# Optimization experiments

Hardware: AMD Instinct MI355X
Metric: run time of the kernel (lower is better)

## Reference

```python
import jax, jax.numpy as jnp
import numpy as np

N = 8192
IN_C = 256
OUT_C = 64
ALPHA = 0.2  # LeakyReLU negative slope
NEG_INF = -9e15


def setup_inputs() -> dict:
    key = jax.random.key(0)
    k1, k2, k3, k4 = jax.random.split(key, 4)
    x = jax.random.normal(k1, (N, IN_C), dtype=jnp.float32)
    adjacent = jax.random.randint(k2, (N, N), 0, 2, dtype=jnp.int32)
    # xavier_uniform with gain=1.2: limit = gain * sqrt(6/(fan_in+fan_out))
    lim_w = 1.2 * np.sqrt(6.0 / (IN_C + OUT_C))
    w = jax.random.uniform(k3, (IN_C, OUT_C), dtype=jnp.float32, minval=-lim_w, maxval=lim_w)
    lim_a = 1.2 * np.sqrt(6.0 / (2 * OUT_C + 1))
    a = jax.random.uniform(k4, (2 * OUT_C, 1), dtype=jnp.float32, minval=-lim_a, maxval=lim_a)
    return {"x": x, "adjacent": adjacent, "w": w, "a": a}


def reference(x, adjacent, w, a):
    # h: [N, out]
    h = x @ w
    # e_ij = LeakyReLU(a^T [h_i || h_j]) computed without materializing [N,N,2*out]:
    # split a into source/target halves -> rank-1 broadcast sum.
    a_src = a[:OUT_C, 0]   # [out]
    a_dst = a[OUT_C:, 0]   # [out]
    f_src = h @ a_src      # [N]
    f_dst = h @ a_dst      # [N]
    e = f_src[:, None] + f_dst[None, :]            # [N, N]
    e = jnp.where(e > 0, e, ALPHA * e)             # LeakyReLU
    # mask by adjacency, softmax over neighbors (rows)
    e = jnp.where(adjacent > 0, e, NEG_INF)
    attention = jax.nn.softmax(e, axis=-1)         # [N, N]
    h_prime = attention @ h                        # [N, out]
    # concat=True -> ELU activation
    return jax.nn.elu(h_prime)
```

## Files before the change

### kernel.cpp

```cpp
#include <hip/hip_runtime.h>
#include <hip/hip_bf16.h>

#define N 8192
#define IN_C 256
#define OUT_C 64
#define ALPHA 0.2f

typedef short bf16x8 __attribute__((ext_vector_type(8)));
typedef float f32x4 __attribute__((ext_vector_type(4)));

#define OFF_H      0u
#define OFF_HT     2097152u
#define OFF_FS     3145728u
#define OFF_FD     3178496u
#define OFF_FDMAX  3211264u
#define OFF_NUM    3211520u

__global__ __launch_bounds__(256) void k_linear(const float* __restrict__ x,
                                                const float* __restrict__ w,
                                                const float* __restrict__ a,
                                                float* __restrict__ h,
                                                float* __restrict__ fs,
                                                float* __restrict__ fd) {
    __shared__ float wl[IN_C * OUT_C];
    int t = threadIdx.x;
    for (int idx = t; idx < IN_C * OUT_C; idx += 256) wl[idx] = w[idx];
    __syncthreads();
    int i = blockIdx.x * 4 + (t >> 6);
    int c = t & 63;
    const float* xr = x + (size_t)i * IN_C;
    float acc = 0.f;
#pragma unroll 8
    for (int k = 0; k < IN_C; ++k) acc = fmaf(xr[k], wl[k * 64 + c], acc);
    h[(size_t)i * 64 + c] = acc;
    float s = acc * a[c];
    float d = acc * a[64 + c];
#pragma unroll
    for (int off = 32; off > 0; off >>= 1) {
        s += __shfl_xor(s, off, 64);
        d += __shfl_xor(d, off, 64);
    }
    if (c == 0) { fs[i] = s; fd[i] = d; }
}

__global__ __launch_bounds__(256) void k_tr(const float* __restrict__ h,
                                            __hip_bfloat16* __restrict__ ht) {
    __shared__ __hip_bfloat16 lds[64 * 65];
    int t = threadIdx.x;
    int i0 = blockIdx.x * 64;
#pragma unroll
    for (int k = 0; k < 16; ++k) {
        int idx = k * 256 + t;
        int il = idx >> 6, c = idx & 63;
        lds[c * 65 + il] = __float2bfloat16(h[(size_t)(i0 + il) * 64 + c]);
    }
    __syncthreads();
#pragma unroll
    for (int k = 0; k < 16; ++k) {
        int idx = k * 256 + t;
        int c = idx >> 6, il = idx & 63;
        ht[(size_t)c * N + i0 + il] = lds[c * 65 + il];
    }
}

__global__ __launch_bounds__(256) void k_fdmax(const float* __restrict__ fd,
                                               float* __restrict__ out) {
    __shared__ float red[256];
    int t = threadIdx.x;
    float m = -3.4e38f;
    for (int j = t; j < N; j += 256) m = fmaxf(m, fd[j]);
    red[t] = m;
    __syncthreads();
    for (int s = 128; s > 0; s >>= 1) {
        if (t < s) red[t] = fmaxf(red[t], red[t + s]);
        __syncthreads();
    }
    if (t == 0) out[0] = red[0];
}

struct Stage {
    int4   ad0, ad1;
    float4 fd0, fd1;
    bf16x8 b0, b1, b2, b3;
};

__device__ __forceinline__ void load_stage(Stage& s,
        const int* __restrict__ arow, const float* __restrict__ fdst,
        const unsigned short* __restrict__ pb0, const unsigned short* __restrict__ pb1,
        const unsigned short* __restrict__ pb2, const unsigned short* __restrict__ pb3,
        int jb) {
    s.ad0 = *(const int4*)(arow + jb);
    s.ad1 = *(const int4*)(arow + jb + 4);
    s.fd0 = *(const float4*)(fdst + jb);
    s.fd1 = *(const float4*)(fdst + jb + 4);
    s.b0  = *(const bf16x8*)(pb0 + jb);
    s.b1  = *(const bf16x8*)(pb1 + jb);
    s.b2  = *(const bf16x8*)(pb2 + jb);
    s.b3  = *(const bf16x8*)(pb3 + jb);
}

__device__ __forceinline__ void compute_stage(const Stage& s, float fs, float m,
        float& dacc, f32x4& acc0, f32x4& acc1, f32x4& acc2, f32x4& acc3) {
    int   ad[8]  = {s.ad0.x, s.ad0.y, s.ad0.z, s.ad0.w, s.ad1.x, s.ad1.y, s.ad1.z, s.ad1.w};
    float fdv[8] = {s.fd0.x, s.fd0.y, s.fd0.z, s.fd0.w, s.fd1.x, s.fd1.y, s.fd1.z, s.fd1.w};
    bf16x8 af;
#pragma unroll
    for (int e = 0; e < 8; ++e) {
        float ee = fs + fdv[e];
        float l  = fmaxf(ee, ALPHA * ee);
        float wt = (ad[e] > 0) ? __expf(l - m) : 0.f;
        dacc += wt;
        union { float f; unsigned u; } cv; cv.f = wt;
        unsigned ru = cv.u + 0x7FFF + ((cv.u >> 16) & 1);
        af[e] = (short)(ru >> 16);
    }
    acc0 = __builtin_amdgcn_mfma_f32_16x16x32_bf16(af, s.b0, acc0, 0, 0, 0);
    acc1 = __builtin_amdgcn_mfma_f32_16x16x32_bf16(af, s.b1, acc1, 0, 0, 0);
    acc2 = __builtin_amdgcn_mfma_f32_16x16x32_bf16(af, s.b2, acc2, 0, 0, 0);
    acc3 = __builtin_amdgcn_mfma_f32_16x16x32_bf16(af, s.b3, acc3, 0, 0, 0);
}

__global__ __launch_bounds__(256) void k_main(
    const int* __restrict__ adj,
    const float* __restrict__ fsrc,
    const float* __restrict__ fdst,
    const float* __restrict__ fdmax_p,
    const unsigned short* __restrict__ ht,
    float* __restrict__ nump,
    float* __restrict__ denp_out,
    int jch, int ns) {
    int bid = blockIdx.x;
    int rb = bid & 127;
    int kq = bid >> 7;
    int t = threadIdx.x;
    int wave = t >> 6;
    int lane = t & 63;
    int r  = lane & 15;
    int kg = lane >> 4;
    int i  = rb * 64 + wave * 16 + r;
    int j0 = kq * jch;

    float fs  = fsrc[i];
    float fdm = *fdmax_p;
    float e0  = fs + fdm;
    float m   = fmaxf(e0, ALPHA * e0);

    const int* arow = adj + (size_t)i * N;
    const unsigned short* pb0 = ht + (size_t)(r)      * N;
    const unsigned short* pb1 = ht + (size_t)(16 + r) * N;
    const unsigned short* pb2 = ht + (size_t)(32 + r) * N;
    const unsigned short* pb3 = ht + (size_t)(48 + r) * N;

    f32x4 acc0 = {0.f,0.f,0.f,0.f}, acc1 = {0.f,0.f,0.f,0.f};
    f32x4 acc2 = {0.f,0.f,0.f,0.f}, acc3 = {0.f,0.f,0.f,0.f};
    float dacc = 0.f;

    int base = j0 + kg * 8;
    Stage A, B;
    load_stage(A, arow, fdst, pb0, pb1, pb2, pb3, base);
    load_stage(B, arow, fdst, pb0, pb1, pb2, pb3, base + 32);

#pragma unroll 1
    for (int ks = 0; ks < ns - 2; ks += 2) {
        compute_stage(A, fs, m, dacc, acc0, acc1, acc2, acc3);
        load_stage(A, arow, fdst, pb0, pb1, pb2, pb3, base + (ks + 2) * 32);
        compute_stage(B, fs, m, dacc, acc0, acc1, acc2, acc3);
        load_stage(B, arow, fdst, pb0, pb1, pb2, pb3, base + (ks + 3) * 32);
    }
    compute_stage(A, fs, m, dacc, acc0, acc1, acc2, acc3);
    compute_stage(B, fs, m, dacc, acc0, acc1, acc2, acc3);

    dacc += __shfl_xor(dacc, 16, 64);
    dacc += __shfl_xor(dacc, 32, 64);
    if (kg == 0) denp_out[kq * N + i] = dacc;

    int orow = rb * 64 + wave * 16 + kg * 4;
    float* np = nump + (size_t)kq * N * 64;
#pragma unroll
    for (int rr = 0; rr < 4; ++rr) {
        np[(size_t)(orow + rr) * 64 + 0 * 16 + r] = acc0[rr];
        np[(size_t)(orow + rr) * 64 + 1 * 16 + r] = acc1[rr];
        np[(size_t)(orow + rr) * 64 + 2 * 16 + r] = acc2[rr];
        np[(size_t)(orow + rr) * 64 + 3 * 16 + r] = acc3[rr];
    }
}

__global__ __launch_bounds__(256) void k_final(const float* __restrict__ nump,
                                               const float* __restrict__ denp,
                                               float* __restrict__ out,
                                               int kqn) {
    int gid = blockIdx.x * 256 + threadIdx.x;
    int i = gid >> 6;
    float num = 0.f, den = 0.f;
    for (int q = 0; q < kqn; ++q) {
        num += nump[(size_t)q * (N * 64) + gid];
        den += denp[q * N + i];
    }
    float v = num / den;
    out[gid] = v > 0.f ? v : __expf(v) - 1.f;
}

extern "C" void kernel_launch(void* const* d_in, const int* in_sizes, int n_in,
                              void* d_out, int out_size, void* d_ws, size_t ws_size,
                              hipStream_t stream) {
    const float* x   = (const float*)d_in[0];
    const int*   adj = (const int*)d_in[1];
    const float* w   = (const float*)d_in[2];
    const float* a   = (const float*)d_in[3];
    float* out = (float*)d_out;
    char*  ws  = (char*)d_ws;

    float*          h    = (float*)(ws + OFF_H);
    __hip_bfloat16* ht   = (__hip_bfloat16*)(ws + OFF_HT);
    float*          fs   = (float*)(ws + OFF_FS);
    float*          fd   = (float*)(ws + OFF_FD);
    float*          fdm  = (float*)(ws + OFF_FDMAX);
    float*          nump = (float*)(ws + OFF_NUM);

    size_t need8 = (size_t)OFF_NUM + 8ull * N * 64 * 4 + 8ull * N * 4;
    int KQ = (ws_size >= need8) ? 8 : 4;
    float* denp = nump + (size_t)KQ * N * 64;
    int jch = N / KQ;
    int ns  = jch / 32;

    k_linear<<<2048, 256, 0, stream>>>(x, w, a, h, fs, fd);
    k_tr<<<128, 256, 0, stream>>>(h, ht);
    k_fdmax<<<1, 256, 0, stream>>>(fd, fdm);
    k_main<<<KQ * 128, 256, 0, stream>>>(adj, fs, fd, fdm,
                                         (const unsigned short*)ht, nump, denp, jch, ns);
    k_final<<<2048, 256, 0, stream>>>(nump, denp, out, KQ);
}
```

Baseline: 469.9 us.

## Compute softmax denominator via ones-MFMA, use exp2 intrinsic, vectorize final kernel

The main kernel no longer accumulates the softmax denominator with scalar adds and cross-lane shuffles. It adds a fifth MFMA against a vector of bf16 ones, so the denominator comes from the same bf16-rounded weights as the numerator. The exponential now uses a pre-scaled log2e fma plus the hardware exp2, the weights go through the library bf16 conversion, and launch bounds ask for 4 waves per SIMD. The final kernel handles four outputs per thread with float4 loads and one reciprocal, trading an extra MFMA per step and possible register pressure for fewer VALU operations.

Result: no change. 468.7 us (-0.3%).

```diff
diff --git a/kernel.cpp b/kernel.cpp
--- a/kernel.cpp
+++ b/kernel.cpp
@@ -5,6 +5,7 @@
 #define IN_C 256
 #define OUT_C 64
 #define ALPHA 0.2f
+#define L2E 1.44269504f
 
 typedef short bf16x8 __attribute__((ext_vector_type(8)));
 typedef float f32x4 __attribute__((ext_vector_type(4)));
@@ -99,8 +100,9 @@
     s.b3  = *(const bf16x8*)(pb3 + jb);
 }
 
-__device__ __forceinline__ void compute_stage(const Stage& s, float fs, float m,
-        float& dacc, f32x4& acc0, f32x4& acc1, f32x4& acc2, f32x4& acc3) {
+__device__ __forceinline__ void compute_stage(const Stage& s, float fs, float mL,
+        const bf16x8& bones,
+        f32x4& acc0, f32x4& acc1, f32x4& acc2, f32x4& acc3, f32x4& acc4) {
     int   ad[8]  = {s.ad0.x, s.ad0.y, s.ad0.z, s.ad0.w, s.ad1.x, s.ad1.y, s.ad1.z, s.ad1.w};
     float fdv[8] = {s.fd0.x, s.fd0.y, s.fd0.z, s.fd0.w, s.fd1.x, s.fd1.y, s.fd1.z, s.fd1.w};
     bf16x8 af;
@@ -108,19 +110,21 @@
     for (int e = 0; e < 8; ++e) {
         float ee = fs + fdv[e];
         float l  = fmaxf(ee, ALPHA * ee);
-        float wt = (ad[e] > 0) ? __expf(l - m) : 0.f;
-        dacc += wt;
-        union { float f; unsigned u; } cv; cv.f = wt;
-        unsigned ru = cv.u + 0x7FFF + ((cv.u >> 16) & 1);
-        af[e] = (short)(ru >> 16);
+        float a2 = __builtin_fmaf(l, L2E, -mL);
+        float wt = __builtin_amdgcn_exp2f(a2);
+        wt = (ad[e] > 0) ? wt : 0.f;
+        __hip_bfloat16 hb = __float2bfloat16(wt);
+        union { __hip_bfloat16 b; short s16; } u; u.b = hb;
+        af[e] = u.s16;
     }
     acc0 = __builtin_amdgcn_mfma_f32_16x16x32_bf16(af, s.b0, acc0, 0, 0, 0);
     acc1 = __builtin_amdgcn_mfma_f32_16x16x32_bf16(af, s.b1, acc1, 0, 0, 0);
     acc2 = __builtin_amdgcn_mfma_f32_16x16x32_bf16(af, s.b2, acc2, 0, 0, 0);
     acc3 = __builtin_amdgcn_mfma_f32_16x16x32_bf16(af, s.b3, acc3, 0, 0, 0);
-}
-
-__global__ __launch_bounds__(256) void k_main(
+    acc4 = __builtin_amdgcn_mfma_f32_16x16x32_bf16(af, bones, acc4, 0, 0, 0);
+}
+
+__global__ __launch_bounds__(256, 4) void k_main(
     const int* __restrict__ adj,
     const float* __restrict__ fsrc,
     const float* __restrict__ fdst,
@@ -144,6 +148,7 @@
     float fdm = *fdmax_p;
     float e0  = fs + fdm;
     float m   = fmaxf(e0, ALPHA * e0);
+    float mL  = m * L2E;
 
     const int* arow = adj + (size_t)i * N;
     const unsigned short* pb0 = ht + (size_t)(r)      * N;
@@ -151,9 +156,13 @@
     const unsigned short* pb2 = ht + (size_t)(32 + r) * N;
     const unsigned short* pb3 = ht + (size_t)(48 + r) * N;
 
+    bf16x8 bones;
+#pragma unroll
+    for (int e = 0; e < 8; ++e) bones[e] = (short)0x3F80;
+
     f32x4 acc0 = {0.f,0.f,0.f,0.f}, acc1 = {0.f,0.f,0.f,0.f};
     f32x4 acc2 = {0.f,0.f,0.f,0.f}, acc3 = {0.f,0.f,0.f,0.f};
-    float dacc = 0.f;
+    f32x4 acc4 = {0.f,0.f,0.f,0.f};
 
     int base = j0 + kg * 8;
     Stage A, B;
@@ -162,17 +171,13 @@
 
 #pragma unroll 1
     for (int ks = 0; ks < ns - 2; ks += 2) {
-        compute_stage(A, fs, m, dacc, acc0, acc1, acc2, acc3);
+        compute_stage(A, fs, mL, bones, acc0, acc1, acc2, acc3, acc4);
         load_stage(A, arow, fdst, pb0, pb1, pb2, pb3, base + (ks + 2) * 32);
-        compute_stage(B, fs, m, dacc, acc0, acc1, acc2, acc3);
+        compute_stage(B, fs, mL, bones, acc0, acc1, acc2, acc3, acc4);
         load_stage(B, arow, fdst, pb0, pb1, pb2, pb3, base + (ks + 3) * 32);
     }
-    compute_stage(A, fs, m, dacc, acc0, acc1, acc2, acc3);
-    compute_stage(B, fs, m, dacc, acc0, acc1, acc2, acc3);
-
-    dacc += __shfl_xor(dacc, 16, 64);
-    dacc += __shfl_xor(dacc, 32, 64);
-    if (kg == 0) denp_out[kq * N + i] = dacc;
+    compute_stage(A, fs, mL, bones, acc0, acc1, acc2, acc3, acc4);
+    compute_stage(B, fs, mL, bones, acc0, acc1, acc2, acc3, acc4);
 
     int orow = rb * 64 + wave * 16 + kg * 4;
     float* np = nump + (size_t)kq * N * 64;
@@ -183,6 +188,10 @@
         np[(size_t)(orow + rr) * 64 + 2 * 16 + r] = acc2[rr];
         np[(size_t)(orow + rr) * 64 + 3 * 16 + r] = acc3[rr];
     }
+    if (r == 0) {
+#pragma unroll
+        for (int rr = 0; rr < 4; ++rr) denp_out[kq * N + orow + rr] = acc4[rr];
+    }
 }
 
 __global__ __launch_bounds__(256) void k_final(const float* __restrict__ nump,
@@ -190,14 +199,23 @@
                                                float* __restrict__ out,
                                                int kqn) {
     int gid = blockIdx.x * 256 + threadIdx.x;
-    int i = gid >> 6;
-    float num = 0.f, den = 0.f;
+    int base = gid * 4;
+    int i = base >> 6;
+    float4 num = {0.f, 0.f, 0.f, 0.f};
+    float den = 0.f;
     for (int q = 0; q < kqn; ++q) {
-        num += nump[(size_t)q * (N * 64) + gid];
+        float4 v = *(const float4*)(nump + (size_t)q * (N * 64) + base);
+        num.x += v.x; num.y += v.y; num.z += v.z; num.w += v.w;
         den += denp[q * N + i];
     }
-    float v = num / den;
-    out[gid] = v > 0.f ? v : __expf(v) - 1.f;
+    float rd = 1.f / den;
+    float4 o;
+    o.x = num.x * rd; o.y = num.y * rd; o.z = num.z * rd; o.w = num.w * rd;
+    o.x = o.x > 0.f ? o.x : __expf(o.x) - 1.f;
+    o.y = o.y > 0.f ? o.y : __expf(o.y) - 1.f;
+    o.z = o.z > 0.f ? o.z : __expf(o.z) - 1.f;
+    o.w = o.w > 0.f ? o.w : __expf(o.w) - 1.f;
+    *(float4*)(out + base) = o;
 }
 
 extern "C" void kernel_launch(void* const* d_in, const int* in_sizes, int n_in,
@@ -228,5 +246,5 @@
     k_fdmax<<<1, 256, 0, stream>>>(fd, fdm);
     k_main<<<KQ * 128, 256, 0, stream>>>(adj, fs, fd, fdm,
                                          (const unsigned short*)ht, nump, denp, jch, ns);
-    k_final<<<2048, 256, 0, stream>>>(nump, denp, out, KQ);
-}
+    k_final<<<512, 256, 0, stream>>>(nump, denp, out, KQ);
+}
```
